# Performance work log

Measured on AMD Instinct MI355X. Metric: run time of the kernel, lower is better.

Reference implementation:

```python
import jax, jax.numpy as jnp
import numpy as np

B, L, E, H = 4, 2048, 1024, 16
HD = E // H  # head_dim = 64


def setup_inputs() -> dict:
    key = jax.random.key(0)
    ks = jax.random.split(key, 11)
    s = 1.0 / np.sqrt(E)
    return {
        "q": jax.random.normal(ks[0], (B, L, E), jnp.float32),
        "k": jax.random.normal(ks[1], (B, L, E), jnp.float32),
        "v": jax.random.normal(ks[2], (B, L, E), jnp.float32),
        "Wq": jax.random.normal(ks[3], (E, E), jnp.float32) * s,
        "bq": jax.random.normal(ks[4], (E,), jnp.float32) * s,
        "Wk": jax.random.normal(ks[5], (E, E), jnp.float32) * s,
        "bk": jax.random.normal(ks[6], (E,), jnp.float32) * s,
        "Wv": jax.random.normal(ks[7], (E, E), jnp.float32) * s,
        "bv": jax.random.normal(ks[8], (E,), jnp.float32) * s,
        "Wo": jax.random.normal(ks[9], (E, E), jnp.float32) * s,
        "bo": jax.random.normal(ks[10], (E,), jnp.float32) * s,
    }


def reference(q, k, v, Wq, bq, Wk, bk, Wv, bv, Wo, bo):
    # Linear projections (torch Linear: x @ W.T + b)
    qp = q @ Wq.T + bq  # [B, L, E]
    kp = k @ Wk.T + bk
    vp = v @ Wv.T + bv
    # split heads -> [B, H, L, HD]
    qh = qp.reshape(B, L, H, HD).transpose(0, 2, 1, 3)
    kh = kp.reshape(B, L, H, HD).transpose(0, 2, 1, 3)
    vh = vp.reshape(B, L, H, HD).transpose(0, 2, 1, 3)
    scale = 1.0 / jnp.sqrt(jnp.asarray(HD, qh.dtype))
    score = jnp.einsum("bhqd,bhkd->bhqk", qh, kh) * scale  # [B, H, L, L]
    attn = jax.nn.softmax(score, axis=-1)
    # dropout p=0 (eval) -> identity
    out = jnp.einsum("bhqk,bhkd->bhqd", attn, vh)  # [B, H, L, HD]
    out = out.transpose(0, 2, 1, 3).reshape(B, L, E)
    out = out @ Wo.T + bo
    # original returns attn flattened over (B*H); match that shape
    return out, attn.reshape(B * H, L, L)
```

## Files before the change

### kernel.cpp

```cpp
#include <hip/hip_runtime.h>
#include <stdint.h>

typedef __attribute__((ext_vector_type(8))) short bf16x8;
typedef __attribute__((ext_vector_type(4))) float f32x4;

#define DEV __device__ __forceinline__

static constexpr int Bsz = 4, Lsz = 2048, Esz = 1024, Hsz = 16, HDsz = 64;
static constexpr int BL = Bsz * Lsz;
static constexpr size_t PLANE = (size_t)BL * Esz;

DEV unsigned short f2bf(float x) {
  union { float f; unsigned u; } c; c.f = x;
  unsigned u = c.u + 0x7FFFu + ((c.u >> 16) & 1u);
  return (unsigned short)(u >> 16);
}
DEV float bf2f(unsigned short h) {
  union { unsigned u; float f; } c; c.u = ((unsigned)h) << 16; return c.f;
}
DEV bf16x8 ld_bf8(const unsigned short* p) { return *(const bf16x8*)p; }

template<bool A_F32, bool W_SPLIT, bool OUT_F32>
__global__ __launch_bounds__(256) void gemm_nt(
    const void* __restrict__ Aptr, const float* __restrict__ W,
    const float* __restrict__ bias, void* __restrict__ Cptr)
{
  constexpr int Kdim = Esz, Ndim = Esz;
  __shared__ unsigned short As[128][40];
  __shared__ unsigned short Bs[W_SPLIT ? 2 : 1][128][40];

  const int t = threadIdx.x;
  const int lane = t & 63, wave = t >> 6;
  const int wr = wave >> 1, wc = wave & 1;
  const int frow = lane & 15, fg = lane >> 4;

  const int f = blockIdx.x + 8 * blockIdx.y;
  const int m_t = ((f & 7) << 3) + (f >> 6);
  const int n_t = (f >> 3) & 7;
  const int m0 = m_t * 128, n0 = n_t * 128;

  f32x4 acc[4][4];
#pragma unroll
  for (int i = 0; i < 4; i++)
#pragma unroll
    for (int j = 0; j < 4; j++) acc[i][j] = f32x4{0.f, 0.f, 0.f, 0.f};

  for (int k0 = 0; k0 < Kdim; k0 += 32) {
    __syncthreads();
#pragma unroll
    for (int j = 0; j < 4; j++) {
      int s = t + j * 256, row = s >> 3, c4 = s & 7;
      if constexpr (A_F32) {
        const float* A = (const float*)Aptr;
        float4 v = *(const float4*)&A[(size_t)(m0 + row) * Kdim + k0 + c4 * 4];
        ushort4 hi;
        hi.x = f2bf(v.x); hi.y = f2bf(v.y); hi.z = f2bf(v.z); hi.w = f2bf(v.w);
        *(ushort4*)&As[row][c4 * 4] = hi;
      } else {
        const unsigned short* A = (const unsigned short*)Aptr;
        *(ushort4*)&As[row][c4 * 4] =
            *(const ushort4*)&A[(size_t)(m0 + row) * Kdim + k0 + c4 * 4];
      }
      {
        float4 v = *(const float4*)&W[(size_t)(n0 + row) * Kdim + k0 + c4 * 4];
        ushort4 hi;
        hi.x = f2bf(v.x); hi.y = f2bf(v.y); hi.z = f2bf(v.z); hi.w = f2bf(v.w);
        *(ushort4*)&Bs[0][row][c4 * 4] = hi;
        if constexpr (W_SPLIT) {
          ushort4 lo;
          lo.x = f2bf(v.x - bf2f(hi.x));
          lo.y = f2bf(v.y - bf2f(hi.y));
          lo.z = f2bf(v.z - bf2f(hi.z));
          lo.w = f2bf(v.w - bf2f(hi.w));
          *(ushort4*)&Bs[W_SPLIT ? 1 : 0][row][c4 * 4] = lo;
        }
      }
    }
    __syncthreads();

    bf16x8 ah[4], bhv[4], blv[4];
#pragma unroll
    for (int x = 0; x < 4; x++) {
      ah[x] = ld_bf8(&As[wr * 64 + x * 16 + frow][fg * 8]);
      bhv[x] = ld_bf8(&Bs[0][wc * 64 + x * 16 + frow][fg * 8]);
      if constexpr (W_SPLIT)
        blv[x] = ld_bf8(&Bs[W_SPLIT ? 1 : 0][wc * 64 + x * 16 + frow][fg * 8]);
    }
#pragma unroll
    for (int mi = 0; mi < 4; mi++)
#pragma unroll
      for (int ni = 0; ni < 4; ni++) {
        acc[mi][ni] = __builtin_amdgcn_mfma_f32_16x16x32_bf16(ah[mi], bhv[ni], acc[mi][ni], 0, 0, 0);
        if constexpr (W_SPLIT)
          acc[mi][ni] = __builtin_amdgcn_mfma_f32_16x16x32_bf16(ah[mi], blv[ni], acc[mi][ni], 0, 0, 0);
      }
  }

#pragma unroll
  for (int mi = 0; mi < 4; mi++)
#pragma unroll
    for (int ni = 0; ni < 4; ni++) {
      int col = n0 + wc * 64 + ni * 16 + frow;
      float bv = bias[col];
#pragma unroll
      for (int r = 0; r < 4; r++) {
        int row = m0 + wr * 64 + mi * 16 + fg * 4 + r;
        float val = acc[mi][ni][r] + bv;
        size_t idx = (size_t)row * Ndim + col;
        if constexpr (OUT_F32) ((float*)Cptr)[idx] = val;
        else                   ((unsigned short*)Cptr)[idx] = f2bf(val);
      }
    }
}

__global__ __launch_bounds__(256) void attn_fused(
    const unsigned short* __restrict__ qph, const unsigned short* __restrict__ kph,
    const unsigned short* __restrict__ vp,
    float* __restrict__ attn, unsigned short* __restrict__ oh)
{
  __shared__ unsigned short QP[64][72];
  __shared__ unsigned short Kh[64][72];
  __shared__ unsigned short Vt[64][72];

  const int t = threadIdx.x, lane = t & 63, wave = t >> 6;
  const int frow = lane & 15, fg = lane >> 4;

  const int f = blockIdx.x + 32 * blockIdx.y;
  const int bh = ((f & 7) << 3) + (f >> 8);
  const int qt = (f >> 3) & 31;
  const int b = bh >> 4, h = bh & 15;
  const int q0 = qt * 64;
  const int qw = q0 + wave * 16;

  const size_t base = (size_t)b * Lsz * Esz + (size_t)h * HDsz;
  constexpr float SC2 = 0.1803368801f;

  const int srow = t >> 4, sc4 = (t & 15) * 4;
  const int vrow = t >> 4, vc = t & 15;

  auto loadKh = [&](ushort4* r, int row0) {
#pragma unroll
    for (int j = 0; j < 4; j++)
      r[j] = *(const ushort4*)&kph[base + (size_t)(row0 + srow + j * 16) * Esz + sc4];
  };
  auto writeK = [&](const ushort4* r) {
#pragma unroll
    for (int j = 0; j < 4; j++)
      *(ushort4*)&Kh[srow + j * 16][sc4] = r[j];
  };
  auto loadV = [&](unsigned short (*rv)[4], int row0) {
#pragma unroll
    for (int j = 0; j < 4; j++) {
      size_t g = base + (size_t)(row0 + vrow + j * 16) * Esz + vc;
#pragma unroll
      for (int i = 0; i < 4; i++) rv[j][i] = vp[g + i * 16];
    }
  };
  auto writeV = [&](unsigned short (*rv)[4]) {
#pragma unroll
    for (int j = 0; j < 4; j++) {
#pragma unroll
      for (int i = 0; i < 4; i++) Vt[vc + i * 16][vrow + j * 16] = rv[j][i];
    }
  };

#pragma unroll
  for (int j = 0; j < 4; j++) {
    size_t g = base + (size_t)(q0 + srow + j * 16) * Esz + sc4;
    *(ushort4*)&QP[srow + j * 16][sc4] = *(const ushort4*)&qph[g];
  }
  __syncthreads();
  bf16x8 qfh[2];
#pragma unroll
  for (int dh = 0; dh < 2; dh++)
    qfh[dh] = ld_bf8(&QP[wave * 16 + frow][dh * 32 + fg * 8]);

  float zl[4];
#pragma unroll
  for (int r = 0; r < 4; r++) zl[r] = 0.f;

  auto computeA = [&]() {
#pragma unroll
    for (int kc = 0; kc < 4; kc++) {
      f32x4 sv = f32x4{0.f, 0.f, 0.f, 0.f};
#pragma unroll
      for (int dh = 0; dh < 2; dh++) {
        bf16x8 kf = ld_bf8(&Kh[kc * 16 + frow][dh * 32 + fg * 8]);
        sv = __builtin_amdgcn_mfma_f32_16x16x32_bf16(qfh[dh], kf, sv, 0, 0, 0);
      }
#pragma unroll
      for (int r = 0; r < 4; r++) zl[r] += exp2f(sv[r] * SC2);
    }
  };

  {
    ushort4 rA[4], rB[4];
    loadKh(rA, 0);
    for (int kt = 0; kt < 32; kt += 2) {
      __syncthreads();
      writeK(rA);
      if (kt + 1 < 32) loadKh(rB, (kt + 1) * 64);
      __syncthreads();
      computeA();
      __syncthreads();
      writeK(rB);
      if (kt + 2 < 32) loadKh(rA, (kt + 2) * 64);
      __syncthreads();
      computeA();
    }
  }
  float rz[4];
#pragma unroll
  for (int r = 0; r < 4; r++) {
    float z = zl[r];
#pragma unroll
    for (int o = 1; o < 16; o <<= 1) z += __shfl_xor(z, o);
    rz[r] = 1.f / z;
  }

  f32x4 oacc[4];
#pragma unroll
  for (int d = 0; d < 4; d++) oacc[d] = f32x4{0.f, 0.f, 0.f, 0.f};

  const size_t arow = (size_t)bh * Lsz * Lsz;

  auto computeB = [&](int kt) {
    f32x4 sv[4];
#pragma unroll
    for (int kc = 0; kc < 4; kc++) {
      sv[kc] = f32x4{0.f, 0.f, 0.f, 0.f};
#pragma unroll
      for (int dh = 0; dh < 2; dh++) {
        bf16x8 kfh = ld_bf8(&Kh[kc * 16 + frow][dh * 32 + fg * 8]);
        sv[kc] = __builtin_amdgcn_mfma_f32_16x16x32_bf16(qfh[dh], kfh, sv[kc], 0, 0, 0);
      }
    }
#pragma unroll
    for (int kc = 0; kc < 4; kc++) {
#pragma unroll
      for (int r = 0; r < 4; r++) {
        float p = exp2f(sv[kc][r] * SC2) * rz[r];
        int qrow = qw + fg * 4 + r;
        __builtin_nontemporal_store(p, &attn[arow + (size_t)qrow * Lsz + kt * 64 + kc * 16 + frow]);
        QP[wave * 16 + fg * 4 + r][kc * 16 + frow] = f2bf(p);
      }
    }
    __syncthreads();
#pragma unroll
    for (int kh2 = 0; kh2 < 2; kh2++) {
      bf16x8 pa = ld_bf8(&QP[wave * 16 + frow][kh2 * 32 + fg * 8]);
#pragma unroll
      for (int d = 0; d < 4; d++) {
        bf16x8 vb = ld_bf8(&Vt[d * 16 + frow][kh2 * 32 + fg * 8]);
        oacc[d] = __builtin_amdgcn_mfma_f32_16x16x32_bf16(pa, vb, oacc[d], 0, 0, 0);
      }
    }
  };

  {
    ushort4 khA[4], khB[4];
    unsigned short vA[4][4], vB[4][4];
    loadKh(khA, 0);
    loadV(vA, 0);
    for (int kt = 0; kt < 32; kt += 2) {
      __syncthreads();
      writeK(khA);
      writeV(vA);
      if (kt + 1 < 32) {
        loadKh(khB, (kt + 1) * 64);
        loadV(vB, (kt + 1) * 64);
      }
      __syncthreads();
      computeB(kt);
      __syncthreads();
      writeK(khB);
      writeV(vB);
      if (kt + 2 < 32) {
        loadKh(khA, (kt + 2) * 64);
        loadV(vA, (kt + 2) * 64);
      }
      __syncthreads();
      computeB(kt + 1);
    }
  }

#pragma unroll
  for (int d = 0; d < 4; d++)
#pragma unroll
    for (int r = 0; r < 4; r++) {
      int qrow = qw + fg * 4 + r;
      __builtin_nontemporal_store(f2bf(oacc[d][r]),
          &oh[base + (size_t)qrow * Esz + d * 16 + frow]);
    }
}

extern "C" void kernel_launch(void* const* d_in, const int* in_sizes, int n_in,
                              void* d_out, int out_size, void* d_ws, size_t ws_size,
                              hipStream_t stream)
{
  (void)in_sizes; (void)n_in; (void)out_size; (void)ws_size;

  const float* q  = (const float*)d_in[0];
  const float* k  = (const float*)d_in[1];
  const float* v  = (const float*)d_in[2];
  const float* Wq = (const float*)d_in[3];
  const float* bq = (const float*)d_in[4];
  const float* Wk = (const float*)d_in[5];
  const float* bk = (const float*)d_in[6];
  const float* Wv = (const float*)d_in[7];
  const float* bv = (const float*)d_in[8];
  const float* Wo = (const float*)d_in[9];
  const float* bo = (const float*)d_in[10];

  float* out  = (float*)d_out;
  float* attn = out + PLANE;

  unsigned short* qph = (unsigned short*)d_ws;
  unsigned short* kph = qph + PLANE;
  unsigned short* vpp = kph + PLANE;
  unsigned short* oh  = vpp + PLANE;

  dim3 gg(8, 64), bb(256);
  gemm_nt<true, false, false><<<gg, bb, 0, stream>>>(q, Wq, bq, qph);
  gemm_nt<true, false, false><<<gg, bb, 0, stream>>>(k, Wk, bk, kph);
  gemm_nt<true, false, false><<<gg, bb, 0, stream>>>(v, Wv, bv, vpp);

  dim3 ga(32, 64);
  attn_fused<<<ga, bb, 0, stream>>>(qph, kph, vpp, attn, oh);

  gemm_nt<false, true, true><<<gg, bb, 0, stream>>>(oh, Wo, bo, out);
}
```

Before: 519.6 us.

## Vectorize attention-probability stores via LDS staging and halve syncs in normalizer pass

The attention-matrix write now goes through the bf16 probability tile already staged in LDS. Each lane writes a contiguous 16-byte float4 row segment instead of scattered scalar stores, which should improve coalescing of the large attn output. The normalizer pass also stages two K tiles at once, using the Vt buffer as a second K buffer, so there are two barriers per 128 keys instead of four. The stored attention values are now rounded through bf16, which adds precision loss to the returned attn matrix.

```diff
diff --git a/kernel.cpp b/kernel.cpp
--- a/kernel.cpp
+++ b/kernel.cpp
@@ -143,10 +143,10 @@
     for (int j = 0; j < 4; j++)
       r[j] = *(const ushort4*)&kph[base + (size_t)(row0 + srow + j * 16) * Esz + sc4];
   };
-  auto writeK = [&](const ushort4* r) {
+  auto writeK = [&](unsigned short (*dst)[72], const ushort4* r) {
 #pragma unroll
     for (int j = 0; j < 4; j++)
-      *(ushort4*)&Kh[srow + j * 16][sc4] = r[j];
+      *(ushort4*)&dst[srow + j * 16][sc4] = r[j];
   };
   auto loadV = [&](unsigned short (*rv)[4], int row0) {
 #pragma unroll
@@ -179,13 +179,13 @@
 #pragma unroll
   for (int r = 0; r < 4; r++) zl[r] = 0.f;
 
-  auto computeA = [&]() {
+  auto computeA = [&](unsigned short (*Kc)[72]) {
 #pragma unroll
     for (int kc = 0; kc < 4; kc++) {
       f32x4 sv = f32x4{0.f, 0.f, 0.f, 0.f};
 #pragma unroll
       for (int dh = 0; dh < 2; dh++) {
-        bf16x8 kf = ld_bf8(&Kh[kc * 16 + frow][dh * 32 + fg * 8]);
+        bf16x8 kf = ld_bf8(&Kc[kc * 16 + frow][dh * 32 + fg * 8]);
         sv = __builtin_amdgcn_mfma_f32_16x16x32_bf16(qfh[dh], kf, sv, 0, 0, 0);
       }
 #pragma unroll
@@ -196,17 +196,18 @@
   {
     ushort4 rA[4], rB[4];
     loadKh(rA, 0);
+    loadKh(rB, 64);
     for (int kt = 0; kt < 32; kt += 2) {
       __syncthreads();
-      writeK(rA);
-      if (kt + 1 < 32) loadKh(rB, (kt + 1) * 64);
-      __syncthreads();
-      computeA();
-      __syncthreads();
-      writeK(rB);
-      if (kt + 2 < 32) loadKh(rA, (kt + 2) * 64);
-      __syncthreads();
-      computeA();
+      writeK(Kh, rA);
+      writeK(Vt, rB);
+      if (kt + 2 < 32) {
+        loadKh(rA, (kt + 2) * 64);
+        loadKh(rB, (kt + 3) * 64);
+      }
+      __syncthreads();
+      computeA(Kh);
+      computeA(Vt);
     }
   }
   float rz[4];
@@ -240,12 +241,20 @@
 #pragma unroll
       for (int r = 0; r < 4; r++) {
         float p = exp2f(sv[kc][r] * SC2) * rz[r];
-        int qrow = qw + fg * 4 + r;
-        __builtin_nontemporal_store(p, &attn[arow + (size_t)qrow * Lsz + kt * 64 + kc * 16 + frow]);
         QP[wave * 16 + fg * 4 + r][kc * 16 + frow] = f2bf(p);
       }
     }
     __syncthreads();
+#pragma unroll
+    for (int it = 0; it < 4; it++) {
+      int prow = it * 4 + fg;
+      int pc = frow * 4;
+      ushort4 pv4 = *(const ushort4*)&QP[wave * 16 + prow][pc];
+      f32x4 w;
+      w[0] = bf2f(pv4.x); w[1] = bf2f(pv4.y); w[2] = bf2f(pv4.z); w[3] = bf2f(pv4.w);
+      __builtin_nontemporal_store(w,
+          (f32x4*)&attn[arow + (size_t)(qw + prow) * Lsz + kt * 64 + pc]);
+    }
 #pragma unroll
     for (int kh2 = 0; kh2 < 2; kh2++) {
       bf16x8 pa = ld_bf8(&QP[wave * 16 + frow][kh2 * 32 + fg * 8]);
@@ -264,7 +273,7 @@
     loadV(vA, 0);
     for (int kt = 0; kt < 32; kt += 2) {
       __syncthreads();
-      writeK(khA);
+      writeK(Kh, khA);
       writeV(vA);
       if (kt + 1 < 32) {
         loadKh(khB, (kt + 1) * 64);
@@ -273,7 +282,7 @@
       __syncthreads();
       computeB(kt);
       __syncthreads();
-      writeK(khB);
+      writeK(Kh, khB);
       writeV(vB);
       if (kt + 2 < 32) {
         loadKh(khA, (kt + 2) * 64);
```

Result: faster. 475.1 us (-8.6%).
